# Kernel tuning notes

Hardware: AMD Instinct MI355X
Metric: run time of the kernel (lower is better)

The kernel has to match this reference:

```python
import jax, jax.numpy as jnp
import numpy as np
from jax import lax

NDEMOG, IC, OC, KS = 4, 128, 256, 3
B, H, W = 64, 56, 56


def setup_inputs() -> dict:
    key = jax.random.key(0)
    k1, k2, k3, k4 = jax.random.split(key, 4)
    x = jax.random.normal(k1, (B, IC, H, W), dtype=jnp.float32)
    demog_label = jax.random.randint(k2, (B,), 0, NDEMOG, dtype=jnp.int32)
    kernel_base = jax.random.normal(k3, (OC, IC, KS, KS), dtype=jnp.float32) * 0.05
    kernel_mask = jax.random.uniform(k4, (NDEMOG, IC, KS, KS), dtype=jnp.float32)
    return {"x": x, "demog_label": demog_label, "kernel_base": kernel_base,
            "kernel_mask": kernel_mask, "epoch": 5}


def _conv(x, k):
    # NCHW / OIHW, stride=1, padding=1 (same as F.conv2d(stride=1, padding=1))
    return lax.conv_general_dilated(
        x, k, window_strides=(1, 1), padding=[(1, 1), (1, 1)],
        dimension_numbers=("NCHW", "OIHW", "NCHW"))


def reference(x, demog_label, kernel_base, kernel_mask, epoch):
    # epoch (=5) < fuse_epoch (=9) in the original module, so the per-demographic
    # mask kernel_mask[d] is always used. The torch code gathers the samples of
    # each demographic group, convolves with kernel_base * mask[d], and scatters
    # results back. Equivalent fused form: conv the full batch with each masked
    # kernel and select per-sample by demog_label (ndemog is a small constant).
    ndemog = kernel_mask.shape[0]
    out = jnp.zeros((x.shape[0], kernel_base.shape[0], x.shape[2], x.shape[3]), x.dtype)
    for d in range(ndemog):
        k = kernel_base * kernel_mask[d][None]          # [OC, IC, KS, KS]
        y = _conv(x, k)                                  # [B, OC, H, W]
        sel = (demog_label == d)[:, None, None, None]
        out = out + jnp.where(sel, y, jnp.zeros((), x.dtype))
    return out
```

## Files before the change

kernel.cpp:

```cpp
#include <hip/hip_runtime.h>


typedef __bf16 v8bf __attribute__((ext_vector_type(8)));
typedef float  v4f  __attribute__((ext_vector_type(4)));
typedef unsigned short v8us __attribute__((ext_vector_type(8)));

#define IC_  128
#define OC_  256
#define HH   56
#define WW_  56
#define HW_  3136
#define PW   58
#define XP_PER_B (PW * PW * IC_)
#define WQ_ELEMS (4 * 9 * OC_ * IC_)

__device__ __forceinline__ unsigned short f2bf(float f) {
    unsigned u = __builtin_bit_cast(unsigned, f);
    u += 0x7fffu + ((u >> 16) & 1u);
    return (unsigned short)(u >> 16);
}

typedef __attribute__((address_space(3))) unsigned int lds_u32_t;
typedef const __attribute__((address_space(1))) unsigned int gbl_u32_t;

__device__ __forceinline__ void gload_lds16(const unsigned short* gsrc, unsigned short* ldst) {
    __builtin_amdgcn_global_load_lds((gbl_u32_t*)gsrc,
                                     (lds_u32_t*)(unsigned int)(unsigned long long)(uintptr_t)ldst,
                                     16, 0, 0);
}

__global__ __launch_bounds__(256)
void transpose_pad(const float* __restrict__ x, unsigned short* __restrict__ xp)
{
    __shared__ unsigned short lt[IC_ * 58];
    const int blk = blockIdx.x;
    const int b = blk / HH, h = blk % HH;
    const int t = threadIdx.x;
    const float* xb = x + (size_t)b * IC_ * HW_ + h * WW_;
    #pragma unroll
    for (int i = 0; i < 7; ++i) {
        int e4 = t + i * 256;
        int ic = e4 / 14;
        int w4 = (e4 - ic * 14) * 4;
        v4f v = *(const v4f*)&xb[ic * HW_ + w4];
        unsigned lo = (unsigned)f2bf(v[0]) | ((unsigned)f2bf(v[1]) << 16);
        unsigned hi = (unsigned)f2bf(v[2]) | ((unsigned)f2bf(v[3]) << 16);
        unsigned* dst = (unsigned*)&lt[ic * 58 + w4];
        dst[0] = lo;
        dst[1] = hi;
    }
    __syncthreads();
    unsigned short* xpb = xp + (size_t)b * XP_PER_B + (size_t)(h + 1) * PW * IC_;
    #pragma unroll
    for (int i = 0; i < 4; ++i) {
        int s = t + i * 256;
        if (s < 896) {
            int w = s >> 4, icg = s & 15;
            unsigned short v[8];
            #pragma unroll
            for (int j = 0; j < 8; ++j) v[j] = lt[(icg * 8 + j) * 58 + w];
            *(v8us*)&xpb[(w + 1) * IC_ + icg * 8] = *(const v8us*)v;
        }
    }
    if (t < 32) {
        int col = (t >> 4) * 57;
        *(v8us*)&xpb[(size_t)col * IC_ + (t & 15) * 8] = (v8us)(unsigned short)0;
    }
    if (h == 0 || h == HH - 1) {
        unsigned short* row = xp + (size_t)b * XP_PER_B + (h == 0 ? 0 : (size_t)(PW - 1) * PW * IC_);
        for (int s = t; s < 928; s += 256)
            *(v8us*)&row[(size_t)s * 8] = (v8us)(unsigned short)0;
    }
}

__global__ __launch_bounds__(256)
void build_weights(const float* __restrict__ kbase, const float* __restrict__ kmask,
                   unsigned short* __restrict__ wq)
{
    int t  = blockIdx.x * 256 + threadIdx.x;
    int ic = t & 127;
    int oc = (t >> 7) & 255;
    int rd = t >> 15;
    int r  = rd % 9, d = rd / 9;
    float v = kbase[oc * 1152 + ic * 9 + r] * kmask[d * 1152 + ic * 9 + r];
    wq[t] = f2bf(v);
}

__global__ __launch_bounds__(256, 4)
void adaconv_main(const unsigned short* __restrict__ xp,
                  const unsigned short* __restrict__ wq,
                  const int* __restrict__ demog,
                  float* __restrict__ out)
{
    __shared__ unsigned short lds_a[2][64 * 32];
    __shared__ unsigned short lds_b[2][256 * 32];

    const int t    = threadIdx.x;
    const int lane = t & 63;
    const int quad = lane >> 4;
    const int l15  = lane & 15;
    const int wid  = __builtin_amdgcn_readfirstlane(t >> 6);

    const int mtile = blockIdx.x;
    const int b     = blockIdx.y;
    const int p0    = mtile * 64;
    const int d     = demog[b];

    const int spix = p0 + (t >> 2);
    const int sh   = spix / WW_;
    const int sw   = spix - sh * WW_;
    const unsigned short* asrc = xp + (size_t)b * XP_PER_B
                               + (size_t)((sh + 1) * PW + (sw + 1)) * IC_ + (t & 3) * 8;
    const unsigned short* bsrc = wq + (size_t)d * 9 * OC_ * IC_
                               + (t >> 2) * IC_ + (t & 3) * 8;

    v4f acc[4][4];
    #pragma unroll
    for (int mi = 0; mi < 4; ++mi)
        #pragma unroll
        for (int ni = 0; ni < 4; ++ni)
            acc[mi][ni] = (v4f)0.0f;

    #define STAGE(buf, c)                                                              \
        do {                                                                           \
            const int r_   = (c) >> 2;                                                 \
            const int icb_ = (c) & 3;                                                  \
            const int toff_ = ((r_ / 3 - 1) * PW + (r_ % 3 - 1)) * IC_;                \
            const int ic0_  = icb_ * 32;                                               \
            gload_lds16(asrc + toff_ + ic0_, &lds_a[(buf)][wid * 512]);                \
            _Pragma("unroll")                                                          \
            for (int j = 0; j < 4; ++j)                                                \
                gload_lds16(bsrc + r_ * (OC_ * IC_) + j * 64 * IC_ + ic0_,             \
                            &lds_b[(buf)][wid * 512 + j * 2048]);                      \
        } while (0)

    STAGE(0, 0);
    __syncthreads();

    #pragma unroll
    for (int c = 0; c < 36; ++c) {
        const int cur = c & 1;
        if (c + 1 < 36) STAGE(cur ^ 1, c + 1);

        v8us au[4], bu[4];
        #pragma unroll
        for (int mi = 0; mi < 4; ++mi)
            au[mi] = *(const v8us*)&lds_a[cur][(mi * 16 + l15) * 32 + quad * 8];
        #pragma unroll
        for (int ni = 0; ni < 4; ++ni)
            bu[ni] = *(const v8us*)&lds_b[cur][(wid * 64 + ni * 16 + l15) * 32 + quad * 8];

        #pragma unroll
        for (int mi = 0; mi < 4; ++mi) {
            v8bf a = __builtin_bit_cast(v8bf, au[mi]);
            #pragma unroll
            for (int ni = 0; ni < 4; ++ni) {
                v8bf bb = __builtin_bit_cast(v8bf, bu[ni]);
                acc[mi][ni] = __builtin_amdgcn_mfma_f32_16x16x32_bf16(a, bb, acc[mi][ni], 0, 0, 0);
            }
        }
        __syncthreads();
    }
    #undef STAGE

    float* ob = out + ((size_t)b * OC_ + wid * 64) * HW_ + p0;
    #pragma unroll
    for (int ni = 0; ni < 4; ++ni) {
        #pragma unroll
        for (int mi = 0; mi < 4; ++mi) {
            float* o = ob + (size_t)(ni * 16 + l15) * HW_ + mi * 16 + quad * 4;
            *(v4f*)o = acc[mi][ni];
        }
    }
}

extern "C" void kernel_launch(void* const* d_in, const int* in_sizes, int n_in,
                              void* d_out, int out_size, void* d_ws, size_t ws_size,
                              hipStream_t stream) {
    const float* x     = (const float*)d_in[0];
    const int*   demog = (const int*)d_in[1];
    const float* kbase = (const float*)d_in[2];
    const float* kmask = (const float*)d_in[3];
    float* out = (float*)d_out;

    unsigned short* xp = (unsigned short*)d_ws;
    unsigned short* wq = xp + (size_t)64 * XP_PER_B;
    transpose_pad<<<64 * HH, 256, 0, stream>>>(x, xp);
    build_weights<<<WQ_ELEMS / 256, 256, 0, stream>>>(kbase, kmask, wq);
    adaconv_main<<<dim3(49, 64), 256, 0, stream>>>(xp, wq, demog, out);
}
```

Before: 449.5 us.

## Stage input halo rows once in swizzled LDS and read weights directly into registers

The main conv kernel now loads the padded input rows covering each 64-pixel tile (with halo) into LDS once per 64-channel half, using an XOR swizzle, and forms all 9 taps from that shared tile instead of restaging A for every tap. Weights are no longer staged through LDS. Each wave loads its B fragments straight from global memory into double-buffered registers, which drops the per-iteration barriers. This cuts redundant input traffic and sync overhead, but raises register pressure (launch bounds lowered to 3) and leaves the weight loads exposed to global latency.

```diff
diff --git a/kernel.cpp b/kernel.cpp
--- a/kernel.cpp
+++ b/kernel.cpp
@@ -86,14 +86,13 @@
     wq[t] = f2bf(v);
 }
 
-__global__ __launch_bounds__(256, 4)
+__global__ __launch_bounds__(256, 3)
 void adaconv_main(const unsigned short* __restrict__ xp,
                   const unsigned short* __restrict__ wq,
                   const int* __restrict__ demog,
                   float* __restrict__ out)
 {
-    __shared__ unsigned short lds_a[2][64 * 32];
-    __shared__ unsigned short lds_b[2][256 * 32];
+    __shared__ unsigned short lds_x[232 * 64];
 
     const int t    = threadIdx.x;
     const int lane = t & 63;
@@ -105,14 +104,23 @@
     const int b     = blockIdx.y;
     const int p0    = mtile * 64;
     const int d     = demog[b];
-
-    const int spix = p0 + (t >> 2);
-    const int sh   = spix / WW_;
-    const int sw   = spix - sh * WW_;
-    const unsigned short* asrc = xp + (size_t)b * XP_PER_B
-                               + (size_t)((sh + 1) * PW + (sw + 1)) * IC_ + (t & 3) * 8;
-    const unsigned short* bsrc = wq + (size_t)d * 9 * OC_ * IC_
-                               + (t >> 2) * IC_ + (t & 3) * 8;
+    const int h0    = p0 / WW_;
+
+    int baseR[4];
+    #pragma unroll
+    for (int mi = 0; mi < 4; ++mi) {
+        int pix = p0 + mi * 16 + l15;
+        int hh  = pix / WW_;
+        int wwp = pix - hh * WW_;
+        baseR[mi] = (hh - h0 + 1) * PW + (wwp + 1);
+    }
+
+    const int olane = ((lane >> 3) << 7) + ((((lane & 7) ^ (lane >> 3))) << 3);
+
+    const unsigned short* bbase[4];
+    #pragma unroll
+    for (int ni = 0; ni < 4; ++ni)
+        bbase[ni] = wq + (size_t)d * 9 * OC_ * IC_ + (size_t)(wid * 64 + ni * 16 + l15) * IC_ + quad * 8;
 
     v4f acc[4][4];
     #pragma unroll
@@ -121,47 +129,65 @@
         for (int ni = 0; ni < 4; ++ni)
             acc[mi][ni] = (v4f)0.0f;
 
-    #define STAGE(buf, c)                                                              \
-        do {                                                                           \
-            const int r_   = (c) >> 2;                                                 \
-            const int icb_ = (c) & 3;                                                  \
-            const int toff_ = ((r_ / 3 - 1) * PW + (r_ % 3 - 1)) * IC_;                \
-            const int ic0_  = icb_ * 32;                                               \
-            gload_lds16(asrc + toff_ + ic0_, &lds_a[(buf)][wid * 512]);                \
-            _Pragma("unroll")                                                          \
-            for (int j = 0; j < 4; ++j)                                                \
-                gload_lds16(bsrc + r_ * (OC_ * IC_) + j * 64 * IC_ + ic0_,             \
-                            &lds_b[(buf)][wid * 512 + j * 2048]);                      \
+    int tAq[4];
+    v8us au[2][4], bu[2][4];
+
+    #define SETTAP(r)                                                          \
+        do { const int offR_ = ((r) / 3 - 1) * PW + ((r) % 3 - 1);             \
+            _Pragma("unroll") for (int mi = 0; mi < 4; ++mi) {                 \
+                int R_ = baseR[mi] + offR_;                                    \
+                tAq[mi] = (R_ << 7) + (((R_ & 7) ^ quad) << 4);                \
+            } } while (0)
+
+    #define LOADA(buf, il)                                                     \
+        do { _Pragma("unroll") for (int mi = 0; mi < 4; ++mi)                  \
+            au[buf][mi] = *(const v8us*)((const char*)lds_x + (tAq[mi] ^ ((il) << 6))); \
         } while (0)
 
-    STAGE(0, 0);
-    __syncthreads();
-
-    #pragma unroll
-    for (int c = 0; c < 36; ++c) {
-        const int cur = c & 1;
-        if (c + 1 < 36) STAGE(cur ^ 1, c + 1);
-
-        v8us au[4], bu[4];
+    #define LOADB(buf, r, il)                                                  \
+        do { _Pragma("unroll") for (int ni = 0; ni < 4; ++ni)                  \
+            bu[buf][ni] = *(const v8us*)(bbase[ni] + (r) * (OC_ * IC_) + icofs + (il) * 32); \
+        } while (0)
+
+    #pragma unroll
+    for (int half = 0; half < 2; ++half) {
+        const unsigned short* xph = xp + (size_t)b * XP_PER_B
+                                  + (size_t)h0 * PW * IC_ + half * 64;
+        if (half) __syncthreads();
+        for (int k = wid; k < 29; k += 4)
+            gload_lds16(xph + (size_t)k * 1024 + olane, lds_x + k * 512);
+        __syncthreads();
+
+        const int icofs = half * 64;
+
+        SETTAP(0);
+        LOADA(0, 0);
+        LOADB(0, 0, 0);
+
         #pragma unroll
-        for (int mi = 0; mi < 4; ++mi)
-            au[mi] = *(const v8us*)&lds_a[cur][(mi * 16 + l15) * 32 + quad * 8];
-        #pragma unroll
-        for (int ni = 0; ni < 4; ++ni)
-            bu[ni] = *(const v8us*)&lds_b[cur][(wid * 64 + ni * 16 + l15) * 32 + quad * 8];
-
-        #pragma unroll
-        for (int mi = 0; mi < 4; ++mi) {
-            v8bf a = __builtin_bit_cast(v8bf, au[mi]);
+        for (int c = 0; c < 18; ++c) {
+            const int cur = c & 1;
+            const int nc  = c + 1;
+            if (nc < 18) {
+                const int nr = nc >> 1, nil = nc & 1;
+                if (nil == 0) SETTAP(nr);
+                LOADB(cur ^ 1, nr, nil);
+                LOADA(cur ^ 1, nil);
+            }
             #pragma unroll
-            for (int ni = 0; ni < 4; ++ni) {
-                v8bf bb = __builtin_bit_cast(v8bf, bu[ni]);
-                acc[mi][ni] = __builtin_amdgcn_mfma_f32_16x16x32_bf16(a, bb, acc[mi][ni], 0, 0, 0);
+            for (int mi = 0; mi < 4; ++mi) {
+                v8bf a = __builtin_bit_cast(v8bf, au[cur][mi]);
+                #pragma unroll
+                for (int ni = 0; ni < 4; ++ni) {
+                    v8bf bb = __builtin_bit_cast(v8bf, bu[cur][ni]);
+                    acc[mi][ni] = __builtin_amdgcn_mfma_f32_16x16x32_bf16(a, bb, acc[mi][ni], 0, 0, 0);
+                }
             }
         }
-        __syncthreads();
-    }
-    #undef STAGE
+    }
+    #undef SETTAP
+    #undef LOADA
+    #undef LOADB
 
     float* ob = out + ((size_t)b * OC_ + wid * 64) * HW_ + p0;
     #pragma unroll
```

Result: slower. 575.2 us (+28.0%).

## Stage input halo panel once per half and triple-buffer weights with swizzled LDS

Applied to the files above, without the earlier changes.

Instead of re-fetching the shifted A tile for every one of the nine taps, the kernel loads a padded row panel covering the 64-pixel tile plus its halo into LDS once per 64-channel half, and derives each tap's A fragments by address offset. Weights move to a three-deep ring buffer with explicit vmcnt waits and raw barriers so two stages are in flight. LDS layouts are XOR-swizzled to avoid bank conflicts, blocks are remapped across the grid for better L2 locality, and MFMA sections get raised priority. The larger LDS footprint lowers launch bounds from 4 to 2 blocks per CU, trading occupancy for less global and LDS traffic.

```diff
diff --git a/kernel.cpp b/kernel.cpp
--- a/kernel.cpp
+++ b/kernel.cpp
@@ -86,14 +86,14 @@
     wq[t] = f2bf(v);
 }
 
-__global__ __launch_bounds__(256, 4)
+__global__ __launch_bounds__(256, 2)
 void adaconv_main(const unsigned short* __restrict__ xp,
                   const unsigned short* __restrict__ wq,
                   const int* __restrict__ demog,
                   float* __restrict__ out)
 {
-    __shared__ unsigned short lds_a[2][64 * 32];
-    __shared__ unsigned short lds_b[2][256 * 32];
+    __shared__ unsigned short panel[232 * 64];
+    __shared__ unsigned short bbuf[3][256 * 32];
 
     const int t    = threadIdx.x;
     const int lane = t & 63;
@@ -101,18 +101,39 @@
     const int l15  = lane & 15;
     const int wid  = __builtin_amdgcn_readfirstlane(t >> 6);
 
-    const int mtile = blockIdx.x;
-    const int b     = blockIdx.y;
-    const int p0    = mtile * 64;
-    const int d     = demog[b];
-
-    const int spix = p0 + (t >> 2);
-    const int sh   = spix / WW_;
-    const int sw   = spix - sh * WW_;
-    const unsigned short* asrc = xp + (size_t)b * XP_PER_B
-                               + (size_t)((sh + 1) * PW + (sw + 1)) * IC_ + (t & 3) * 8;
-    const unsigned short* bsrc = wq + (size_t)d * 9 * OC_ * IC_
-                               + (t >> 2) * IC_ + (t & 3) * 8;
+    const int lin = blockIdx.y * 49 + blockIdx.x;
+    const int nl  = (lin & 7) * 392 + (lin >> 3);
+    const int mtile = nl % 49;
+    const int b     = nl / 49;
+
+    const int p0 = mtile * 64;
+    const int d  = demog[b];
+    const int h0 = p0 / WW_;
+
+    int baseR[4];
+    #pragma unroll
+    for (int mi = 0; mi < 4; ++mi) {
+        int pix = p0 + mi * 16 + l15;
+        int hh  = pix / WW_;
+        int wwp = pix - hh * WW_;
+        baseR[mi] = (hh - h0 + 1) * PW + (wwp + 1);
+    }
+
+    const int olane = ((lane >> 3) << 7) + (((lane & 7) ^ (lane >> 3)) << 3);
+    const unsigned short* xpb = xp + (size_t)b * XP_PER_B + (size_t)h0 * PW * IC_;
+
+    const int slotp = (lane & 7) ^ (lane >> 3);
+    const int ocb   = 2 * (wid * 8 + (lane >> 3)) + (slotp >> 2);
+    const unsigned short* sB = wq + (size_t)d * 9 * OC_ * IC_
+                             + (size_t)ocb * IC_ + (slotp & 3) * 8;
+
+    int bOff[4];
+    #pragma unroll
+    for (int ni = 0; ni < 4; ++ni) {
+        int oc = wid * 64 + ni * 16 + l15;
+        int r128 = oc >> 1;
+        bOff[ni] = (r128 << 7) + (((((oc & 1) << 2) | quad) ^ (r128 & 7)) << 4);
+    }
 
     v4f acc[4][4];
     #pragma unroll
@@ -121,35 +142,63 @@
         for (int ni = 0; ni < 4; ++ni)
             acc[mi][ni] = (v4f)0.0f;
 
-    #define STAGE(buf, c)                                                              \
-        do {                                                                           \
-            const int r_   = (c) >> 2;                                                 \
-            const int icb_ = (c) & 3;                                                  \
-            const int toff_ = ((r_ / 3 - 1) * PW + (r_ % 3 - 1)) * IC_;                \
-            const int ic0_  = icb_ * 32;                                               \
-            gload_lds16(asrc + toff_ + ic0_, &lds_a[(buf)][wid * 512]);                \
-            _Pragma("unroll")                                                          \
-            for (int j = 0; j < 4; ++j)                                                \
-                gload_lds16(bsrc + r_ * (OC_ * IC_) + j * 64 * IC_ + ic0_,             \
-                            &lds_b[(buf)][wid * 512 + j * 2048]);                      \
+    int tA[4];
+
+    #define STAGEA(half_) do {                                                  \
+        const unsigned short* xph_ = xpb + (half_) * 64;                        \
+        _Pragma("unroll")                                                       \
+        for (int kk = 0; kk < 8; ++kk) {                                        \
+            int k_ = wid + kk * 4;                                              \
+            if (k_ < 29) gload_lds16(xph_ + k_ * 1024 + olane, panel + k_ * 512); \
+        } } while (0)
+
+    #define STAGEB(bufi, c_) do {                                               \
+        const int r_   = ((c_) % 18) >> 1;                                      \
+        const int ic0_ = ((c_) / 18) * 64 + (((c_) % 18) & 1) * 32;             \
+        const unsigned short* s_ = sB + r_ * (OC_ * IC_) + ic0_;                \
+        _Pragma("unroll")                                                       \
+        for (int j = 0; j < 4; ++j)                                             \
+            gload_lds16(s_ + j * 64 * IC_, &bbuf[bufi][wid * 512 + j * 2048]);  \
         } while (0)
 
-    STAGE(0, 0);
-    __syncthreads();
+    #define SETTAP(r_) do {                                                     \
+        const int offR_ = ((r_) / 3 - 1) * PW + ((r_) % 3 - 1);                 \
+        _Pragma("unroll")                                                       \
+        for (int mi = 0; mi < 4; ++mi) {                                        \
+            int R_ = baseR[mi] + offR_;                                         \
+            tA[mi] = (R_ << 7) + (((R_ & 7) ^ quad) << 4);                      \
+        } } while (0)
+
+    STAGEA(0);
+    STAGEB(0, 0);
+    STAGEB(1, 1);
+    asm volatile("s_waitcnt vmcnt(0)" ::: "memory");
+    __builtin_amdgcn_s_barrier();
 
     #pragma unroll
     for (int c = 0; c < 36; ++c) {
-        const int cur = c & 1;
-        if (c + 1 < 36) STAGE(cur ^ 1, c + 1);
+        if (c > 0) {
+            if (c < 35) asm volatile("s_waitcnt vmcnt(4)" ::: "memory");
+            else        asm volatile("s_waitcnt vmcnt(0)" ::: "memory");
+            __builtin_amdgcn_s_barrier();
+        }
+        if (c == 18) STAGEA(1);
+        if (c + 2 < 36) STAGEB((c + 2) % 3, c + 2);
+        if (c == 18) asm volatile("s_waitcnt vmcnt(4)" ::: "memory");
+
+        const int r   = (c % 18) >> 1;
+        const int icb = (c % 18) & 1;
+        if (icb == 0) SETTAP(r);
 
         v8us au[4], bu[4];
         #pragma unroll
         for (int mi = 0; mi < 4; ++mi)
-            au[mi] = *(const v8us*)&lds_a[cur][(mi * 16 + l15) * 32 + quad * 8];
+            au[mi] = *(const v8us*)((const char*)panel + (tA[mi] ^ (icb << 6)));
         #pragma unroll
         for (int ni = 0; ni < 4; ++ni)
-            bu[ni] = *(const v8us*)&lds_b[cur][(wid * 64 + ni * 16 + l15) * 32 + quad * 8];
-
+            bu[ni] = *(const v8us*)((const char*)bbuf[c % 3] + bOff[ni]);
+
+        __builtin_amdgcn_s_setprio(1);
         #pragma unroll
         for (int mi = 0; mi < 4; ++mi) {
             v8bf a = __builtin_bit_cast(v8bf, au[mi]);
@@ -159,9 +208,11 @@
                 acc[mi][ni] = __builtin_amdgcn_mfma_f32_16x16x32_bf16(a, bb, acc[mi][ni], 0, 0, 0);
             }
         }
-        __syncthreads();
-    }
-    #undef STAGE
+        __builtin_amdgcn_s_setprio(0);
+    }
+    #undef STAGEA
+    #undef STAGEB
+    #undef SETTAP
 
     float* ob = out + ((size_t)b * OC_ + wid * 64) * HW_ + p0;
     #pragma unroll
```

After: 420.6 us. 1.07x faster.
